# Performance work log

Measured on AMD Instinct MI355X. Metric: run time of the kernel, lower is better.

The kernel has to match this reference:

```python
import jax, jax.numpy as jnp
import numpy as np

N_NODES = 100000
N_EDGES = 1600000
H = 64
N_LAYERS = 3
NUM_APPS = max(1, N_LAYERS - 1)  # forward applies layer once, then while l>1 loop


def setup_inputs() -> dict:
    key = jax.random.key(0)
    k1, k2, k3, k4, k5 = jax.random.split(key, 5)
    features = jax.random.normal(k1, (N_NODES, H), dtype=jnp.float32)
    W = jax.random.normal(k2, (H, H), dtype=jnp.float32) / np.sqrt(H)
    b = jax.random.normal(k3, (H,), dtype=jnp.float32) * 0.01
    src = jax.random.randint(k4, (N_EDGES,), 0, N_NODES, dtype=jnp.int64)
    dst = jax.random.randint(k5, (N_EDGES,), 0, N_NODES, dtype=jnp.int64)
    return {"features": features, "W": W, "b": b, "src": src, "dst": dst}


def reference(features, W, b, src, dst):
    n = features.shape[0]
    ones = jnp.ones(src.shape[0], dtype=features.dtype)
    # DGL GraphConv norm='both': symmetric normalization, degrees clamped >= 1
    deg_out = jax.ops.segment_sum(ones, src, num_segments=n)
    deg_in = jax.ops.segment_sum(ones, dst, num_segments=n)
    inv_sqrt_out = jnp.clip(deg_out, 1.0, None) ** -0.5  # [N]
    inv_sqrt_in = jnp.clip(deg_in, 1.0, None) ** -0.5    # [N]

    h = features
    for _ in range(NUM_APPS):  # shared-weight GraphConv + ReLU, applied n_layers-1 times
        msg = (h * inv_sqrt_out[:, None])[src]                   # [E, H] gather
        agg = jax.ops.segment_sum(msg, dst, num_segments=n)      # [N, H] scatter-add
        h = jax.nn.relu((agg * inv_sqrt_in[:, None]) @ W + b)    # [N, H]
    return h
```

## Files before the change

### kernel.cpp

```cpp
#include <hip/hip_runtime.h>
#include <hip/hip_fp16.h>

#define N_NODES 100000
#define N_EDGES 1600000
#define HDIM 64
#define NPB 512
#define NPB_SHIFT 9
#define NBUCK 196
#define CAP 16384
#define NCHUNK 256
#define CHUNK (N_EDGES / NCHUNK)

typedef float f4v __attribute__((ext_vector_type(4)));

__global__ void init_kernel(int* __restrict__ gcurD, int* __restrict__ gcurS) {
    int t = threadIdx.x;
    if (t < NBUCK) {
        gcurD[t] = t * CAP;
        gcurS[t] = t * CAP;
    }
}

__device__ inline uint2 f4_to_h4(float x, float y, float z, float w) {
    __half2 lo = __floats2half2_rn(x, y);
    __half2 hi = __floats2half2_rn(z, w);
    uint2 r;
    r.x = *(unsigned*)&lo;
    r.y = *(unsigned*)&hi;
    return r;
}

__device__ __forceinline__ void dense_body(int t, int r0,
                                           const float* __restrict__ h,
                                           const float* __restrict__ W,
                                           uint2* __restrict__ hw, int n) {
    __shared__ float Wlds[HDIM * HDIM];
    __shared__ float Alds[32][HDIM + 1];

    for (int i = t; i < HDIM * HDIM / 4; i += 256)
        ((f4v*)Wlds)[i] = ((const f4v*)W)[i];

    for (int i = t; i < 512; i += 256) {
        int r = i >> 4;
        int c4 = i & 15;
        int row = r0 + r;
        f4v v = {0.f, 0.f, 0.f, 0.f};
        if (row < n)
            v = __builtin_nontemporal_load((const f4v*)h + (long long)row * 16 + c4);
        Alds[r][c4 * 4 + 0] = v.x;
        Alds[r][c4 * 4 + 1] = v.y;
        Alds[r][c4 * 4 + 2] = v.z;
        Alds[r][c4 * 4 + 3] = v.w;
    }
    __syncthreads();

    int tx = t & 15;
    int ty = t >> 4;
    float4 acc0 = make_float4(0.f, 0.f, 0.f, 0.f);
    float4 acc1 = acc0;

#pragma unroll 8
    for (int k = 0; k < HDIM; ++k) {
        f4v w = ((const f4v*)(Wlds + k * HDIM))[tx];
        float a0 = Alds[2 * ty + 0][k];
        float a1 = Alds[2 * ty + 1][k];
        acc0.x = fmaf(a0, w.x, acc0.x); acc0.y = fmaf(a0, w.y, acc0.y);
        acc0.z = fmaf(a0, w.z, acc0.z); acc0.w = fmaf(a0, w.w, acc0.w);
        acc1.x = fmaf(a1, w.x, acc1.x); acc1.y = fmaf(a1, w.y, acc1.y);
        acc1.z = fmaf(a1, w.z, acc1.z); acc1.w = fmaf(a1, w.w, acc1.w);
    }

    int rb = r0 + 2 * ty;
    if (rb + 0 < n) hw[(long long)(rb + 0) * 16 + tx] = f4_to_h4(acc0.x, acc0.y, acc0.z, acc0.w);
    if (rb + 1 < n) hw[(long long)(rb + 1) * 16 + tx] = f4_to_h4(acc1.x, acc1.y, acc1.z, acc1.w);
}

__global__ void place_dense_kernel(const int* __restrict__ src, const int* __restrict__ dst,
                                   int* __restrict__ gcurD, int* __restrict__ gcurS,
                                   unsigned int* __restrict__ bufD, unsigned short* __restrict__ bufS,
                                   const float* __restrict__ h, const float* __restrict__ W,
                                   uint2* __restrict__ hw, int n) {
    int t = threadIdx.x, blk = blockIdx.x;
    if (blk < NCHUNK) {
        __shared__ int hD[NBUCK], hS[NBUCK], curD[NBUCK], curS[NBUCK];
        for (int i = t; i < NBUCK; i += 256) { hD[i] = 0; hS[i] = 0; }
        __syncthreads();
        int e0 = blk * CHUNK;
        for (int i = t; i < CHUNK; i += 256) {
            atomicAdd(&hD[dst[e0 + i] >> NPB_SHIFT], 1);
            atomicAdd(&hS[src[e0 + i] >> NPB_SHIFT], 1);
        }
        __syncthreads();
        for (int i = t; i < NBUCK; i += 256) {
            curD[i] = hD[i] ? atomicAdd(&gcurD[i], hD[i]) : 0;
            curS[i] = hS[i] ? atomicAdd(&gcurS[i], hS[i]) : 0;
        }
        __syncthreads();
        for (int i = t; i < CHUNK; i += 256) {
            int s = src[e0 + i], d = dst[e0 + i];
            int pd = atomicAdd(&curD[d >> NPB_SHIFT], 1);
            bufD[pd] = (unsigned)s | ((unsigned)(d & (NPB - 1)) << 17);
            int ps = atomicAdd(&curS[s >> NPB_SHIFT], 1);
            bufS[ps] = (unsigned short)(s & (NPB - 1));
        }
    } else {
        dense_body(t, (blk - NCHUNK) * 32, h, W, hw, n);
    }
}

__global__ void dense_kernel(const float* __restrict__ h, const float* __restrict__ W,
                             uint2* __restrict__ hw, int n) {
    dense_body(threadIdx.x, blockIdx.x * 32, h, W, hw, n);
}

__global__ void bucket_kernel(const unsigned int* __restrict__ bufD,
                              const unsigned short* __restrict__ bufS,
                              const int* __restrict__ gcurD, const int* __restrict__ gcurS,
                              int* __restrict__ csr_src, int2* __restrict__ offs,
                              float* __restrict__ inv_in, float* __restrict__ inv_out) {
    __shared__ int cnt[NPB], pre[NPB], cur[NPB];
    int t = threadIdx.x;
    int blk = blockIdx.x;
    if (blk < NBUCK) {
        int b = blk;
        int ebase = b * CAP;
        int ecnt  = gcurD[b] - ebase;
        cnt[t] = 0;
        __syncthreads();
        for (int i = t; i < ecnt; i += NPB)
            atomicAdd(&cnt[(int)(bufD[ebase + i] >> 17)], 1);
        __syncthreads();
        int v = cnt[t];
        pre[t] = v;
        __syncthreads();
        for (int off = 1; off < NPB; off <<= 1) {
            int x = (t >= off) ? pre[t - off] : 0;
            __syncthreads(); pre[t] += x; __syncthreads();
        }
        int excl = pre[t] - v;
        cur[t] = excl;
        int node = b * NPB + t;
        if (node < N_NODES) {
            offs[node] = make_int2(ebase + excl, ebase + excl + v);
            inv_in[node] = rsqrtf((float)max(v, 1));
        }
        __syncthreads();
        for (int i = t; i < ecnt; i += NPB) {
            unsigned en = bufD[ebase + i];
            int pos = atomicAdd(&cur[(int)(en >> 17)], 1);
            csr_src[ebase + pos] = (int)(en & 0x1FFFFu);
        }
    } else {
        int b = blk - NBUCK;
        int ebase = b * CAP;
        int ecnt  = gcurS[b] - ebase;
        cnt[t] = 0;
        __syncthreads();
        for (int i = t; i < ecnt; i += NPB)
            atomicAdd(&cnt[(int)bufS[ebase + i]], 1);
        __syncthreads();
        int node = b * NPB + t;
        if (node < N_NODES) inv_out[node] = rsqrtf((float)max(cnt[t], 1));
    }
}

__global__ void gather_kernel(const uint4* __restrict__ hw, const float* __restrict__ inv_in,
                              const float* __restrict__ inv_out,
                              const int2* __restrict__ offs, const int* __restrict__ csr_src,
                              const float* __restrict__ bias, float* __restrict__ out, int n) {
    int t = threadIdx.x;
    int wave = t >> 6, lane = t & 63;
    int g = lane >> 3, gl = lane & 7;
    int row = blockIdx.x * 32 + wave * 8 + g;
    if (row >= n) return;

    float acc0 = 0.f, acc1 = 0.f, acc2 = 0.f, acc3 = 0.f;
    float acc4 = 0.f, acc5 = 0.f, acc6 = 0.f, acc7 = 0.f;

    int2 oe = offs[row];
    int start = oe.x, end = oe.y;
    int gbase = g << 3;

    int jb = start;
    int mm = end - jb; if (mm > 8) mm = 8;
    int sidx = (mm > 0 && gl < mm) ? csr_src[jb + gl] : 0;
    float sw = inv_out[sidx];

    while (jb < end) {
        int jb2 = jb + 8;
        int mm2 = end - jb2; if (mm2 > 8) mm2 = 8;
        int sidx2 = (jb2 < end && gl < mm2) ? csr_src[jb2 + gl] : 0;
        float sw2 = inv_out[sidx2];

        if (mm == 8) {
#pragma unroll
            for (int j = 0; j < 8; ++j) {
                int s = __shfl(sidx, gbase + j, 64);
                float w = __shfl(sw, gbase + j, 64);
                uint4 u = hw[(long long)s * 8 + gl];
                float2 f0 = __half22float2(*(__half2*)&u.x);
                float2 f1 = __half22float2(*(__half2*)&u.y);
                float2 f2 = __half22float2(*(__half2*)&u.z);
                float2 f3 = __half22float2(*(__half2*)&u.w);
                acc0 = fmaf(f0.x, w, acc0); acc1 = fmaf(f0.y, w, acc1);
                acc2 = fmaf(f1.x, w, acc2); acc3 = fmaf(f1.y, w, acc3);
                acc4 = fmaf(f2.x, w, acc4); acc5 = fmaf(f2.y, w, acc5);
                acc6 = fmaf(f3.x, w, acc6); acc7 = fmaf(f3.y, w, acc7);
            }
        } else {
            for (int j = 0; j < mm; ++j) {
                int s = __shfl(sidx, gbase + j, 64);
                float w = __shfl(sw, gbase + j, 64);
                uint4 u = hw[(long long)s * 8 + gl];
                float2 f0 = __half22float2(*(__half2*)&u.x);
                float2 f1 = __half22float2(*(__half2*)&u.y);
                float2 f2 = __half22float2(*(__half2*)&u.z);
                float2 f3 = __half22float2(*(__half2*)&u.w);
                acc0 = fmaf(f0.x, w, acc0); acc1 = fmaf(f0.y, w, acc1);
                acc2 = fmaf(f1.x, w, acc2); acc3 = fmaf(f1.y, w, acc3);
                acc4 = fmaf(f2.x, w, acc4); acc5 = fmaf(f2.y, w, acc5);
                acc6 = fmaf(f3.x, w, acc6); acc7 = fmaf(f3.y, w, acc7);
            }
        }
        jb = jb2; mm = mm2; sidx = sidx2; sw = sw2;
    }

    float sc = inv_in[row];
    float4 b0 = ((const float4*)bias)[gl * 2 + 0];
    float4 b1 = ((const float4*)bias)[gl * 2 + 1];
    f4v r0, r1;
    r0.x = fmaxf(fmaf(acc0, sc, b0.x), 0.f);
    r0.y = fmaxf(fmaf(acc1, sc, b0.y), 0.f);
    r0.z = fmaxf(fmaf(acc2, sc, b0.z), 0.f);
    r0.w = fmaxf(fmaf(acc3, sc, b0.w), 0.f);
    r1.x = fmaxf(fmaf(acc4, sc, b1.x), 0.f);
    r1.y = fmaxf(fmaf(acc5, sc, b1.y), 0.f);
    r1.z = fmaxf(fmaf(acc6, sc, b1.z), 0.f);
    r1.w = fmaxf(fmaf(acc7, sc, b1.w), 0.f);
    __builtin_nontemporal_store(r0, (f4v*)out + (long long)row * 16 + gl * 2 + 0);
    __builtin_nontemporal_store(r1, (f4v*)out + (long long)row * 16 + gl * 2 + 1);
}

extern "C" void kernel_launch(void* const* d_in, const int* in_sizes, int n_in,
                              void* d_out, int out_size, void* d_ws, size_t ws_size,
                              hipStream_t stream) {
    const float* features = (const float*)d_in[0];
    const float* W        = (const float*)d_in[1];
    const float* b        = (const float*)d_in[2];
    const int*   src      = (const int*)d_in[3];
    const int*   dst      = (const int*)d_in[4];

    float* out = (float*)d_out;

    float* ws = (float*)d_ws;
    uint2* hw = (uint2*)ws;
    unsigned int*   bufD = (unsigned int*)(ws + (size_t)N_NODES * 32);
    unsigned short* bufS = (unsigned short*)(bufD + (size_t)NBUCK * CAP);
    int*   csr_src = (int*)(bufS + (size_t)NBUCK * CAP);
    int2*  offs    = (int2*)(csr_src + (size_t)NBUCK * CAP);
    float* inv_out = (float*)(offs + N_NODES);
    float* inv_in  = inv_out + N_NODES;
    int*   gcurD   = (int*)(inv_in + N_NODES);
    int*   gcurS   = gcurD + NBUCK;

    const int N = N_NODES;
    int dense_blocks  = (N + 31) / 32;
    int gather_blocks = (N + 31) / 32;

    init_kernel<<<1, 256, 0, stream>>>(gcurD, gcurS);

    place_dense_kernel<<<NCHUNK + dense_blocks, 256, 0, stream>>>(
        src, dst, gcurD, gcurS, bufD, bufS, features, W, hw, N);

    bucket_kernel<<<2 * NBUCK, NPB, 0, stream>>>(bufD, bufS, gcurD, gcurS,
                                                 csr_src, offs, inv_in, inv_out);

    gather_kernel<<<gather_blocks, 256, 0, stream>>>((const uint4*)hw, inv_in, inv_out,
                                                     offs, csr_src, b, out, N);

    dense_kernel<<<dense_blocks, 256, 0, stream>>>(out, W, hw, N);
    gather_kernel<<<gather_blocks, 256, 0, stream>>>((const uint4*)hw, inv_in, inv_out,
                                                     offs, csr_src, b, out, N);
}
```

Measured before the change: 239.6 us.

## Fuse first-layer gather with next dense matmul, drop fp32 intermediate round-trip

Adds a gather_dense_kernel that does the first layer's neighbour aggregation, scaling, bias and ReLU, then multiplies by W in registers using wave shuffles and writes the fp16 projected features straight to a second buffer. This removes the separate dense kernel launch and the fp32 write and re-read of the intermediate h. The dense body is also rewritten to keep rows in registers and broadcast via __shfl instead of staging the A tile in LDS. In exchange, the fused kernel has no row<n guard, which is safe only because N is a multiple of 32, and it needs an extra workspace buffer.

Measured after the change: 257.9 us. +7.6%, slower.

```diff
diff --git a/kernel.cpp b/kernel.cpp
--- a/kernel.cpp
+++ b/kernel.cpp
@@ -35,44 +35,38 @@
                                            const float* __restrict__ W,
                                            uint2* __restrict__ hw, int n) {
     __shared__ float Wlds[HDIM * HDIM];
-    __shared__ float Alds[32][HDIM + 1];
-
     for (int i = t; i < HDIM * HDIM / 4; i += 256)
         ((f4v*)Wlds)[i] = ((const f4v*)W)[i];
 
-    for (int i = t; i < 512; i += 256) {
-        int r = i >> 4;
-        int c4 = i & 15;
-        int row = r0 + r;
-        f4v v = {0.f, 0.f, 0.f, 0.f};
-        if (row < n)
-            v = __builtin_nontemporal_load((const f4v*)h + (long long)row * 16 + c4);
-        Alds[r][c4 * 4 + 0] = v.x;
-        Alds[r][c4 * 4 + 1] = v.y;
-        Alds[r][c4 * 4 + 2] = v.z;
-        Alds[r][c4 * 4 + 3] = v.w;
+    int r = t >> 3, gl = t & 7;
+    int row = r0 + r;
+    f4v a0 = {0.f, 0.f, 0.f, 0.f}, a1 = a0;
+    if (row < n) {
+        a0 = __builtin_nontemporal_load((const f4v*)h + (long long)row * 16 + gl * 2 + 0);
+        a1 = __builtin_nontemporal_load((const f4v*)h + (long long)row * 16 + gl * 2 + 1);
     }
     __syncthreads();
 
-    int tx = t & 15;
-    int ty = t >> 4;
-    float4 acc0 = make_float4(0.f, 0.f, 0.f, 0.f);
-    float4 acc1 = acc0;
-
-#pragma unroll 8
+    float acc0 = 0.f, acc1 = 0.f, acc2 = 0.f, acc3 = 0.f;
+    float acc4 = 0.f, acc5 = 0.f, acc6 = 0.f, acc7 = 0.f;
+    int gbase = (t & 63) & 56;
+
+#pragma unroll
     for (int k = 0; k < HDIM; ++k) {
-        f4v w = ((const f4v*)(Wlds + k * HDIM))[tx];
-        float a0 = Alds[2 * ty + 0][k];
-        float a1 = Alds[2 * ty + 1][k];
-        acc0.x = fmaf(a0, w.x, acc0.x); acc0.y = fmaf(a0, w.y, acc0.y);
-        acc0.z = fmaf(a0, w.z, acc0.z); acc0.w = fmaf(a0, w.w, acc0.w);
-        acc1.x = fmaf(a1, w.x, acc1.x); acc1.y = fmaf(a1, w.y, acc1.y);
-        acc1.z = fmaf(a1, w.z, acc1.z); acc1.w = fmaf(a1, w.w, acc1.w);
-    }
-
-    int rb = r0 + 2 * ty;
-    if (rb + 0 < n) hw[(long long)(rb + 0) * 16 + tx] = f4_to_h4(acc0.x, acc0.y, acc0.z, acc0.w);
-    if (rb + 1 < n) hw[(long long)(rb + 1) * 16 + tx] = f4_to_h4(acc1.x, acc1.y, acc1.z, acc1.w);
+        float av = ((k >> 2) & 1) ? a1[k & 3] : a0[k & 3];
+        float ak = __shfl(av, gbase + (k >> 3), 64);
+        f4v w0 = ((const f4v*)Wlds)[k * 16 + gl * 2 + 0];
+        f4v w1 = ((const f4v*)Wlds)[k * 16 + gl * 2 + 1];
+        acc0 = fmaf(ak, w0.x, acc0); acc1 = fmaf(ak, w0.y, acc1);
+        acc2 = fmaf(ak, w0.z, acc2); acc3 = fmaf(ak, w0.w, acc3);
+        acc4 = fmaf(ak, w1.x, acc4); acc5 = fmaf(ak, w1.y, acc5);
+        acc6 = fmaf(ak, w1.z, acc6); acc7 = fmaf(ak, w1.w, acc7);
+    }
+
+    if (row < n) {
+        hw[(long long)row * 16 + gl * 2 + 0] = f4_to_h4(acc0, acc1, acc2, acc3);
+        hw[(long long)row * 16 + gl * 2 + 1] = f4_to_h4(acc4, acc5, acc6, acc7);
+    }
 }
 
 __global__ void place_dense_kernel(const int* __restrict__ src, const int* __restrict__ dst,
@@ -106,11 +100,6 @@
     } else {
         dense_body(t, (blk - NCHUNK) * 32, h, W, hw, n);
     }
-}
-
-__global__ void dense_kernel(const float* __restrict__ h, const float* __restrict__ W,
-                             uint2* __restrict__ hw, int n) {
-    dense_body(threadIdx.x, blockIdx.x * 32, h, W, hw, n);
 }
 
 __global__ void bucket_kernel(const unsigned int* __restrict__ bufD,
@@ -162,6 +151,104 @@
         int node = b * NPB + t;
         if (node < N_NODES) inv_out[node] = rsqrtf((float)max(cnt[t], 1));
     }
+}
+
+__global__ void gather_dense_kernel(const uint4* __restrict__ hw_in, const float* __restrict__ inv_in,
+                                    const float* __restrict__ inv_out,
+                                    const int2* __restrict__ offs, const int* __restrict__ csr_src,
+                                    const float* __restrict__ bias, const float* __restrict__ W,
+                                    uint2* __restrict__ hw_out, int n) {
+    __shared__ float Wlds[HDIM * HDIM];
+    int t = threadIdx.x;
+    for (int i = t; i < HDIM * HDIM / 4; i += 256)
+        ((f4v*)Wlds)[i] = ((const f4v*)W)[i];
+
+    int wave = t >> 6, lane = t & 63;
+    int g = lane >> 3, gl = lane & 7;
+    int row = blockIdx.x * 32 + wave * 8 + g;
+
+    float acc0 = 0.f, acc1 = 0.f, acc2 = 0.f, acc3 = 0.f;
+    float acc4 = 0.f, acc5 = 0.f, acc6 = 0.f, acc7 = 0.f;
+
+    int2 oe = offs[row];
+    int start = oe.x, end = oe.y;
+    int gbase = g << 3;
+
+    int jb = start;
+    int mm = end - jb; if (mm > 8) mm = 8;
+    int sidx = (mm > 0 && gl < mm) ? csr_src[jb + gl] : 0;
+    float sw = inv_out[sidx];
+
+    while (jb < end) {
+        int jb2 = jb + 8;
+        int mm2 = end - jb2; if (mm2 > 8) mm2 = 8;
+        int sidx2 = (jb2 < end && gl < mm2) ? csr_src[jb2 + gl] : 0;
+        float sw2 = inv_out[sidx2];
+
+        if (mm == 8) {
+#pragma unroll
+            for (int j = 0; j < 8; ++j) {
+                int s = __shfl(sidx, gbase + j, 64);
+                float w = __shfl(sw, gbase + j, 64);
+                uint4 u = hw_in[(long long)s * 8 + gl];
+                float2 f0 = __half22float2(*(__half2*)&u.x);
+                float2 f1 = __half22float2(*(__half2*)&u.y);
+                float2 f2 = __half22float2(*(__half2*)&u.z);
+                float2 f3 = __half22float2(*(__half2*)&u.w);
+                acc0 = fmaf(f0.x, w, acc0); acc1 = fmaf(f0.y, w, acc1);
+                acc2 = fmaf(f1.x, w, acc2); acc3 = fmaf(f1.y, w, acc3);
+                acc4 = fmaf(f2.x, w, acc4); acc5 = fmaf(f2.y, w, acc5);
+                acc6 = fmaf(f3.x, w, acc6); acc7 = fmaf(f3.y, w, acc7);
+            }
+        } else {
+            for (int j = 0; j < mm; ++j) {
+                int s = __shfl(sidx, gbase + j, 64);
+                float w = __shfl(sw, gbase + j, 64);
+                uint4 u = hw_in[(long long)s * 8 + gl];
+                float2 f0 = __half22float2(*(__half2*)&u.x);
+                float2 f1 = __half22float2(*(__half2*)&u.y);
+                float2 f2 = __half22float2(*(__half2*)&u.z);
+                float2 f3 = __half22float2(*(__half2*)&u.w);
+                acc0 = fmaf(f0.x, w, acc0); acc1 = fmaf(f0.y, w, acc1);
+                acc2 = fmaf(f1.x, w, acc2); acc3 = fmaf(f1.y, w, acc3);
+                acc4 = fmaf(f2.x, w, acc4); acc5 = fmaf(f2.y, w, acc5);
+                acc6 = fmaf(f3.x, w, acc6); acc7 = fmaf(f3.y, w, acc7);
+            }
+        }
+        jb = jb2; mm = mm2; sidx = sidx2; sw = sw2;
+    }
+
+    float sc = inv_in[row];
+    float4 b0 = ((const float4*)bias)[gl * 2 + 0];
+    float4 b1 = ((const float4*)bias)[gl * 2 + 1];
+    f4v h0, h1;
+    h0.x = fmaxf(fmaf(acc0, sc, b0.x), 0.f);
+    h0.y = fmaxf(fmaf(acc1, sc, b0.y), 0.f);
+    h0.z = fmaxf(fmaf(acc2, sc, b0.z), 0.f);
+    h0.w = fmaxf(fmaf(acc3, sc, b0.w), 0.f);
+    h1.x = fmaxf(fmaf(acc4, sc, b1.x), 0.f);
+    h1.y = fmaxf(fmaf(acc5, sc, b1.y), 0.f);
+    h1.z = fmaxf(fmaf(acc6, sc, b1.z), 0.f);
+    h1.w = fmaxf(fmaf(acc7, sc, b1.w), 0.f);
+
+    __syncthreads();
+
+    float d0 = 0.f, d1 = 0.f, d2 = 0.f, d3 = 0.f;
+    float d4 = 0.f, d5 = 0.f, d6 = 0.f, d7 = 0.f;
+#pragma unroll
+    for (int k = 0; k < HDIM; ++k) {
+        float av = ((k >> 2) & 1) ? h1[k & 3] : h0[k & 3];
+        float ak = __shfl(av, gbase + (k >> 3), 64);
+        f4v w0 = ((const f4v*)Wlds)[k * 16 + gl * 2 + 0];
+        f4v w1 = ((const f4v*)Wlds)[k * 16 + gl * 2 + 1];
+        d0 = fmaf(ak, w0.x, d0); d1 = fmaf(ak, w0.y, d1);
+        d2 = fmaf(ak, w0.z, d2); d3 = fmaf(ak, w0.w, d3);
+        d4 = fmaf(ak, w1.x, d4); d5 = fmaf(ak, w1.y, d5);
+        d6 = fmaf(ak, w1.z, d6); d7 = fmaf(ak, w1.w, d7);
+    }
+
+    hw_out[(long long)row * 16 + gl * 2 + 0] = f4_to_h4(d0, d1, d2, d3);
+    hw_out[(long long)row * 16 + gl * 2 + 1] = f4_to_h4(d4, d5, d6, d7);
 }
 
 __global__ void gather_kernel(const uint4* __restrict__ hw, const float* __restrict__ inv_in,
@@ -253,8 +340,9 @@
     float* out = (float*)d_out;
 
     float* ws = (float*)d_ws;
-    uint2* hw = (uint2*)ws;
-    unsigned int*   bufD = (unsigned int*)(ws + (size_t)N_NODES * 32);
+    uint2* hw  = (uint2*)ws;
+    uint2* hw2 = (uint2*)(ws + (size_t)N_NODES * 32);
+    unsigned int*   bufD = (unsigned int*)(ws + (size_t)N_NODES * 64);
     unsigned short* bufS = (unsigned short*)(bufD + (size_t)NBUCK * CAP);
     int*   csr_src = (int*)(bufS + (size_t)NBUCK * CAP);
     int2*  offs    = (int2*)(csr_src + (size_t)NBUCK * CAP);
@@ -275,10 +363,9 @@
     bucket_kernel<<<2 * NBUCK, NPB, 0, stream>>>(bufD, bufS, gcurD, gcurS,
                                                  csr_src, offs, inv_in, inv_out);
 
-    gather_kernel<<<gather_blocks, 256, 0, stream>>>((const uint4*)hw, inv_in, inv_out,
-                                                     offs, csr_src, b, out, N);
-
-    dense_kernel<<<dense_blocks, 256, 0, stream>>>(out, W, hw, N);
-    gather_kernel<<<gather_blocks, 256, 0, stream>>>((const uint4*)hw, inv_in, inv_out,
-                                                     offs, csr_src, b, out, N);
-}
+    gather_dense_kernel<<<gather_blocks, 256, 0, stream>>>(
+        (const uint4*)hw, inv_in, inv_out, offs, csr_src, b, W, hw2, N);
+
+    gather_kernel<<<gather_blocks, 256, 0, stream>>>(
+        (const uint4*)hw2, inv_in, inv_out, offs, csr_src, b, out, N);
+}
```
